# Kernel optimization log

Hardware: AMD Instinct MI355X
Metric: run time of the kernel (lower is better)

The kernel has to match this reference:

```python
import jax, jax.numpy as jnp
import numpy as np
from jax import lax

B, T, D, H = 32, 512, 512, 1024


def setup_inputs() -> dict:
    key = jax.random.key(0)
    ks = jax.random.split(key, 17)
    s_in = 1.0 / np.sqrt(D)
    s_h = 1.0 / np.sqrt(H)
    inp = {"X": jax.random.normal(ks[0], (B, T, D), jnp.float32)}
    names = ["f", "i", "o", "c"]
    for j, n in enumerate(names):
        inp["W" + n] = jax.random.normal(ks[1 + 4 * j], (H, H), jnp.float32) * s_h
        inp["bW" + n] = jax.random.normal(ks[2 + 4 * j], (H,), jnp.float32) * s_h
        inp["U" + n] = jax.random.normal(ks[3 + 4 * j], (H, D), jnp.float32) * s_in
        inp["bU" + n] = jax.random.normal(ks[4 + 4 * j], (H,), jnp.float32) * s_in
    return inp


def reference(X, Wf, bWf, Uf, bUf, Wi, bWi, Ui, bUi, Wo, bWo, Uo, bUo, Wc, bWc, Uc, bUc):
    b, t, d = X.shape
    h_dim = Wf.shape[0]
    # Precompute input projections for all timesteps (batched GEMM): [T, B, H] each
    def in_proj(U, bU):
        return (jnp.einsum("btd,hd->bth", X, U) + bU).transpose(1, 0, 2)

    xf, xi, xo, xc = in_proj(Uf, bUf), in_proj(Ui, bUi), in_proj(Uo, bUo), in_proj(Uc, bUc)

    h0 = jnp.zeros((b, h_dim), X.dtype)
    c0 = jnp.zeros((b, h_dim), X.dtype)

    def step(carry, xs):
        h, c = carry
        xf_t, xi_t, xo_t, xc_t = xs
        f = jax.nn.sigmoid(h @ Wf.T + bWf + xf_t)
        i = jax.nn.sigmoid(h @ Wi.T + bWi + xi_t)
        o = jax.nn.sigmoid(h @ Wo.T + bWo + xo_t)
        c_bar = jnp.tanh(h @ Wc.T + bWc + xc_t)
        c = f * c + i * c_bar
        h = o * jnp.tanh(c)
        return (h, c), h

    (_, _), hs = lax.scan(step, (h0, c0), (xf, xi, xo, xc))  # hs: [T, B, H]
    return hs.transpose(1, 0, 2)  # [B, T, H]
```

## Files before the change

kernel.cpp:

```cpp
#include <hip/hip_runtime.h>
#include <hip/hip_bf16.h>

typedef __bf16 bf16;
typedef __attribute__((ext_vector_type(8))) __bf16 bf16x8;
typedef __attribute__((ext_vector_type(4))) __bf16 bf16x4;
typedef __attribute__((ext_vector_type(4))) float f32x4;
typedef __attribute__((ext_vector_type(4))) unsigned int u32x4;

#define T_STEPS 512
#define NWG 256

#define WS_CNT   0
#define WS_H     4096
#define WS_BTOT  135168
#define WS_XBF   151552
#define WS_BPACK 16928768

__global__ void k_xpack(const float* __restrict__ X, bf16* __restrict__ Xbf) {
    int gid = blockIdx.x * 256 + threadIdx.x;
    int o = gid << 2;
    int d = o & 511, b = (o >> 9) & 31, t = o >> 14;
    const float4 v = *(const float4*)(X + (size_t)(b * 512 + t) * 512 + d);
    bf16x4 r;
    r.x = (bf16)v.x; r.y = (bf16)v.y; r.z = (bf16)v.z; r.w = (bf16)v.w;
    *(bf16x4*)(Xbf + (size_t)(t * 32 + b) * 512 + d) = r;
}

__global__ void k_bpack(const float* __restrict__ W0, const float* __restrict__ W1,
                        const float* __restrict__ W2, const float* __restrict__ W3,
                        const float* __restrict__ U0, const float* __restrict__ U1,
                        const float* __restrict__ U2, const float* __restrict__ U3,
                        bf16* __restrict__ Bp) {
    int gid = blockIdx.x * 256 + threadIdx.x;
    int lane = gid & 63; int idx = gid >> 6;
    int nt = idx & 1;  idx >>= 1;
    int mk = idx % 48; int cg = idx / 48;
    int kbase = mk * 32 + ((lane >> 4) << 3);
    int col = nt * 16 + (lane & 15);
    int g = col >> 3, hl = col & 7;
    int h = cg * 8 + hl;
    const float* Wg = (g == 0) ? W0 : (g == 1) ? W1 : (g == 2) ? W2 : W3;
    const float* Ug = (g == 0) ? U0 : (g == 1) ? U1 : (g == 2) ? U2 : U3;
    const float* src = (kbase < 1024) ? (Wg + (size_t)h * 1024 + kbase)
                                      : (Ug + (size_t)h * 512 + (kbase - 1024));
    float4 v0 = *(const float4*)(src);
    float4 v1 = *(const float4*)(src + 4);
    bf16x8 r;
    r[0] = (bf16)v0.x; r[1] = (bf16)v0.y; r[2] = (bf16)v0.z; r[3] = (bf16)v0.w;
    r[4] = (bf16)v1.x; r[5] = (bf16)v1.y; r[6] = (bf16)v1.z; r[7] = (bf16)v1.w;
    *(bf16x8*)(Bp + (size_t)gid * 8) = r;
}

__global__ void k_init(const float* bWf, const float* bUf, const float* bWi, const float* bUi,
                       const float* bWo, const float* bUo, const float* bWc, const float* bUc,
                       float* btot, bf16* hglob, unsigned* cnt) {
    int gid = blockIdx.x * 256 + threadIdx.x;
    int g = gid >> 10, h = gid & 1023;
    const float* bW = (g == 0) ? bWf : (g == 1) ? bWi : (g == 2) ? bWo : bWc;
    const float* bU = (g == 0) ? bUf : (g == 1) ? bUi : (g == 2) ? bUo : bUc;
    btot[gid] = bW[h] + bU[h];
    uint4 z; z.x = 0u; z.y = 0u; z.z = 0u; z.w = 0u;
    ((uint4*)hglob)[gid] = z;
    ((uint4*)hglob)[gid + 4096] = z;
    if (gid < 1024) cnt[gid] = 0u;
}

#define MFMA(a, b, c) __builtin_amdgcn_mfma_f32_16x16x32_bf16((a), (b), (c), 0, 0, 0)
#define BQ(i) __builtin_bit_cast(bf16x8, bqr[i])

__global__ __launch_bounds__(256, 1) void k_scan(
        const bf16* __restrict__ Bp, const bf16* __restrict__ Xbf,
        const float* __restrict__ btot, bf16* hglob, unsigned* cnt,
        float* __restrict__ out) {
    const int tid = threadIdx.x;
    const int lane = tid & 63, wid = tid >> 6;
    const int wg = blockIdx.x;
    const int p = wg & 1, cg = wg >> 1;

    u32x4 bqr[24];
    {
#pragma unroll
        for (int i = 0; i < 24; ++i) {
            int mk = (i < 16) ? (wid * 8 + (i >> 1)) : (32 + wid * 4 + ((i - 16) >> 1));
            int nt = i & 1;
            const bf16* pfrag = Bp + ((((size_t)(cg * 48 + mk) * 2 + nt) * 64 + lane) << 3);
            asm volatile("global_load_dwordx4 %0, %1, off" : "=v"(bqr[i]) : "v"(pfrag));
        }
        asm volatile("s_waitcnt vmcnt(0)" ::: "memory");
        __builtin_amdgcn_sched_barrier(0);
    }

    const int arow = (lane & 15) + p * 16;
    const int koff = (lane >> 4) << 3;

    const bool ew = tid < 128;
    const int erow = tid & 15;
    const int ehl = (tid >> 4) & 7;
    const int hgl = cg * 8 + ehl;
    float bias0 = 0.f, bias1 = 0.f, bias2 = 0.f, bias3 = 0.f;
    if (ew) {
        bias0 = btot[hgl];
        bias1 = btot[1024 + hgl];
        bias2 = btot[2048 + hgl];
        bias3 = btot[3072 + hgl];
    }
    const int b_glob = p * 16 + erow;
    float* outp = out + (size_t)b_glob * 512 * 1024 + hgl;
    bf16* hstp = hglob + b_glob * 1024 + hgl;
    float cst = 0.f;

    __shared__ float part[4][2][64][4];

    unsigned* root = cnt;
    unsigned* leaf = cnt + 32 + (wg >> 4) * 32;

    for (int t = 0; t < T_STEPS; ++t) {
        f32x4 acc0 = {0.f, 0.f, 0.f, 0.f};
        f32x4 acc1 = {0.f, 0.f, 0.f, 0.f};
        {
            const bf16* xb = Xbf + ((size_t)(t * 32 + arow) << 9) + koff;
#pragma unroll
            for (int m = 0; m < 4; ++m) {
                bf16x8 a = *(const bf16x8*)(xb + ((wid * 4 + m) << 5));
                acc0 = MFMA(a, BQ(16 + 2 * m), acc0);
                acc1 = MFMA(a, BQ(17 + 2 * m), acc1);
            }
        }

        if (t > 0) {
            if (tid == 0) {
                const unsigned target = 16u * (unsigned)t;
                while (__hip_atomic_load(root, __ATOMIC_RELAXED,
                                         __HIP_MEMORY_SCOPE_AGENT) < target)
                    __builtin_amdgcn_s_sleep(1);
            }
            __syncthreads();
        }

        {
            const bf16* hbuf = hglob + ((size_t)(t & 1) << 15) + arow * 1024 + koff;
            u32x4 av[8];
#pragma unroll
            for (int m = 0; m < 8; ++m) {
                const bf16* ph = hbuf + ((wid * 8 + m) << 5);
                asm volatile("global_load_dwordx4 %0, %1, off sc0 sc1"
                             : "=v"(av[m]) : "v"(ph) : "memory");
            }
            asm volatile("s_waitcnt vmcnt(0)" ::: "memory");
            __builtin_amdgcn_sched_barrier(0);
#pragma unroll
            for (int m = 0; m < 8; ++m) {
                bf16x8 a = __builtin_bit_cast(bf16x8, av[m]);
                acc0 = MFMA(a, BQ(2 * m), acc0);
                acc1 = MFMA(a, BQ(2 * m + 1), acc1);
            }
        }
        *(f32x4*)(&part[wid][0][lane][0]) = acc0;
        *(f32x4*)(&part[wid][1][lane][0]) = acc1;
        __syncthreads();

        if (ew) {
            const int li0 = ((erow >> 2) << 4) | ehl;
            const int li1 = li0 | 8;
            const int reg = erow & 3;
            float a0 = bias0, a1 = bias1, a2 = bias2, a3 = bias3;
#pragma unroll
            for (int w = 0; w < 4; ++w) {
                a0 += part[w][0][li0][reg];
                a1 += part[w][0][li1][reg];
                a2 += part[w][1][li0][reg];
                a3 += part[w][1][li1][reg];
            }
            float f  = 1.f / (1.f + __expf(-a0));
            float i  = 1.f / (1.f + __expf(-a1));
            float o  = 1.f / (1.f + __expf(-a2));
            float cb = 2.f / (1.f + __expf(-2.f * a3)) - 1.f;
            cst = f * cst + i * cb;
            float th = 2.f / (1.f + __expf(-2.f * cst)) - 1.f;
            float hv = o * th;
            bf16 hb16 = (bf16)hv;
            unsigned hv32 = (unsigned)__builtin_bit_cast(unsigned short, hb16);
            bf16* hstp_t = hstp + (((t + 1) & 1) << 15);
            asm volatile("global_store_short %0, %1, off sc0 sc1"
                         :: "v"(hstp_t), "v"(hv32) : "memory");
            outp[(size_t)t << 10] = hv;
            asm volatile("s_waitcnt vmcnt(0)" ::: "memory");
        }
        __syncthreads();

        if (t + 1 < T_STEPS && tid == 0) {
            unsigned old = __hip_atomic_fetch_add(leaf, 1u, __ATOMIC_RELAXED,
                                                  __HIP_MEMORY_SCOPE_AGENT);
            if ((old & 15u) == 15u)
                __hip_atomic_fetch_add(root, 1u, __ATOMIC_RELAXED,
                                       __HIP_MEMORY_SCOPE_AGENT);
        }
    }
}

extern "C" void kernel_launch(void* const* d_in, const int* in_sizes, int n_in,
                              void* d_out, int out_size, void* d_ws, size_t ws_size,
                              hipStream_t stream) {
    const float* X   = (const float*)d_in[0];
    const float* Wf  = (const float*)d_in[1];
    const float* bWf = (const float*)d_in[2];
    const float* Uf  = (const float*)d_in[3];
    const float* bUf = (const float*)d_in[4];
    const float* Wi  = (const float*)d_in[5];
    const float* bWi = (const float*)d_in[6];
    const float* Ui  = (const float*)d_in[7];
    const float* bUi = (const float*)d_in[8];
    const float* Wo  = (const float*)d_in[9];
    const float* bWo = (const float*)d_in[10];
    const float* Uo  = (const float*)d_in[11];
    const float* bUo = (const float*)d_in[12];
    const float* Wc  = (const float*)d_in[13];
    const float* bWc = (const float*)d_in[14];
    const float* Uc  = (const float*)d_in[15];
    const float* bUc = (const float*)d_in[16];

    char* ws = (char*)d_ws;
    unsigned* cnt = (unsigned*)(ws + WS_CNT);
    bf16* hglob   = (bf16*)(ws + WS_H);
    float* btot   = (float*)(ws + WS_BTOT);
    bf16* Xbf     = (bf16*)(ws + WS_XBF);
    bf16* Bp      = (bf16*)(ws + WS_BPACK);
    float* out    = (float*)d_out;

    hipLaunchKernelGGL(k_init, dim3(16), dim3(256), 0, stream,
                       bWf, bUf, bWi, bUi, bWo, bUo, bWc, bUc, btot, hglob, cnt);
    hipLaunchKernelGGL(k_xpack, dim3(8192), dim3(256), 0, stream, X, Xbf);
    hipLaunchKernelGGL(k_bpack, dim3(3072), dim3(256), 0, stream,
                       Wf, Wi, Wo, Wc, Uf, Ui, Uo, Uc, Bp);
    hipLaunchKernelGGL(k_scan, dim3(NWG), dim3(256), 0, stream,
                       Bp, Xbf, btot, hglob, cnt, out);
}
```

Measured before the change: 1.841 ms.

## Replace atomic tree barrier with per-wave flag polling and packed h stores

Drops the hierarchical atomic counter barrier. Each wave in the elementwise stage now writes a per-step flag for its batch half, and every wave polls only the 256 flags for its own batch half with vector loads, which removes two __syncthreads per step. The partial-sum buffer is double-buffered so the second block-wide barrier can go. Hidden-state bf16 values are packed with shuffles into 16-byte stores instead of 2-byte scalar stores. The remapped thread layout and the flag scheme change the memory-ordering assumptions, which adds correctness risk.

```diff
diff --git a/kernel.cpp b/kernel.cpp
--- a/kernel.cpp
+++ b/kernel.cpp
@@ -94,8 +94,8 @@
     const int koff = (lane >> 4) << 3;
 
     const bool ew = tid < 128;
-    const int erow = tid & 15;
-    const int ehl = (tid >> 4) & 7;
+    const int erow = (tid >> 3) & 15;
+    const int ehl = tid & 7;
     const int hgl = cg * 8 + ehl;
     float bias0 = 0.f, bias1 = 0.f, bias2 = 0.f, bias3 = 0.f;
     if (ew) {
@@ -106,13 +106,13 @@
     }
     const int b_glob = p * 16 + erow;
     float* outp = out + (size_t)b_glob * 512 * 1024 + hgl;
-    bf16* hstp = hglob + b_glob * 1024 + hgl;
+    bf16* hrow = hglob + b_glob * 1024 + cg * 8;
     float cst = 0.f;
 
-    __shared__ float part[4][2][64][4];
-
-    unsigned* root = cnt;
-    unsigned* leaf = cnt + 32 + (wg >> 4) * 32;
+    __shared__ float part[2][4][2][64][5];
+
+    unsigned* flags = cnt;
+    const unsigned* fpoll = flags + p * 256 + (lane << 2);
 
     for (int t = 0; t < T_STEPS; ++t) {
         f32x4 acc0 = {0.f, 0.f, 0.f, 0.f};
@@ -126,15 +126,18 @@
                 acc1 = MFMA(a, BQ(17 + 2 * m), acc1);
             }
         }
+        __builtin_amdgcn_sched_barrier(0);
 
         if (t > 0) {
-            if (tid == 0) {
-                const unsigned target = 16u * (unsigned)t;
-                while (__hip_atomic_load(root, __ATOMIC_RELAXED,
-                                         __HIP_MEMORY_SCOPE_AGENT) < target)
-                    __builtin_amdgcn_s_sleep(1);
-            }
-            __syncthreads();
+            const unsigned tgt = (unsigned)t;
+            while (true) {
+                u32x4 f;
+                asm volatile("global_load_dwordx4 %0, %1, off sc0 sc1"
+                             : "=v"(f) : "v"(fpoll) : "memory");
+                asm volatile("s_waitcnt vmcnt(0)" ::: "memory");
+                int ok = (f.x >= tgt) && (f.y >= tgt) && (f.z >= tgt) && (f.w >= tgt);
+                if (__all(ok)) break;
+            }
         }
 
         {
@@ -155,21 +158,26 @@
                 acc1 = MFMA(a, BQ(2 * m + 1), acc1);
             }
         }
-        *(f32x4*)(&part[wid][0][lane][0]) = acc0;
-        *(f32x4*)(&part[wid][1][lane][0]) = acc1;
+        {
+            float* pp = &part[t & 1][wid][0][lane][0];
+            pp[0] = acc0.x; pp[1] = acc0.y; pp[2] = acc0.z; pp[3] = acc0.w;
+            float* pq = &part[t & 1][wid][1][lane][0];
+            pq[0] = acc1.x; pq[1] = acc1.y; pq[2] = acc1.z; pq[3] = acc1.w;
+        }
         __syncthreads();
 
         if (ew) {
             const int li0 = ((erow >> 2) << 4) | ehl;
             const int li1 = li0 | 8;
             const int reg = erow & 3;
+            const float (*pt)[2][64][5] = part[t & 1];
             float a0 = bias0, a1 = bias1, a2 = bias2, a3 = bias3;
 #pragma unroll
             for (int w = 0; w < 4; ++w) {
-                a0 += part[w][0][li0][reg];
-                a1 += part[w][0][li1][reg];
-                a2 += part[w][1][li0][reg];
-                a3 += part[w][1][li1][reg];
+                a0 += pt[w][0][li0][reg];
+                a1 += pt[w][0][li1][reg];
+                a2 += pt[w][1][li0][reg];
+                a3 += pt[w][1][li1][reg];
             }
             float f  = 1.f / (1.f + __expf(-a0));
             float i  = 1.f / (1.f + __expf(-a1));
@@ -178,22 +186,32 @@
             cst = f * cst + i * cb;
             float th = 2.f / (1.f + __expf(-2.f * cst)) - 1.f;
             float hv = o * th;
+
             bf16 hb16 = (bf16)hv;
             unsigned hv32 = (unsigned)__builtin_bit_cast(unsigned short, hb16);
-            bf16* hstp_t = hstp + (((t + 1) & 1) << 15);
-            asm volatile("global_store_short %0, %1, off sc0 sc1"
-                         :: "v"(hstp_t), "v"(hv32) : "memory");
+            unsigned w0 = hv32 << ((tid & 1) << 4);
+            w0 |= (unsigned)__shfl_xor((int)w0, 1, 64);
+            unsigned x2 = (unsigned)__shfl_xor((int)w0, 2, 64);
+            unsigned lo2 = (tid & 2) ? x2 : w0;
+            unsigned hi2 = (tid & 2) ? w0 : x2;
+            unsigned xl = (unsigned)__shfl_xor((int)lo2, 4, 64);
+            unsigned xh = (unsigned)__shfl_xor((int)hi2, 4, 64);
+            u32x4 pk;
+            if (tid & 4) { pk.x = xl;  pk.y = xh;  pk.z = lo2; pk.w = hi2; }
+            else         { pk.x = lo2; pk.y = hi2; pk.z = xl;  pk.w = xh; }
+            if (ehl == 0) {
+                bf16* hst = hrow + (((t + 1) & 1) << 15);
+                asm volatile("global_store_dwordx4 %0, %1, off sc0 sc1"
+                             :: "v"(hst), "v"(pk) : "memory");
+            }
             outp[(size_t)t << 10] = hv;
             asm volatile("s_waitcnt vmcnt(0)" ::: "memory");
-        }
-        __syncthreads();
-
-        if (t + 1 < T_STEPS && tid == 0) {
-            unsigned old = __hip_atomic_fetch_add(leaf, 1u, __ATOMIC_RELAXED,
-                                                  __HIP_MEMORY_SCOPE_AGENT);
-            if ((old & 15u) == 15u)
-                __hip_atomic_fetch_add(root, 1u, __ATOMIC_RELAXED,
-                                       __HIP_MEMORY_SCOPE_AGENT);
+            if ((tid & 63) == 0) {
+                unsigned* fl = flags + p * 256 + cg * 2 + (tid >> 6);
+                unsigned v = (unsigned)(t + 1);
+                asm volatile("global_store_dword %0, %1, off sc0 sc1"
+                             :: "v"(fl), "v"(v) : "memory");
+            }
         }
     }
 }
```

Result: slower. 3.182 ms (+72.9%).
